# Kernel optimization log

Hardware: AMD Instinct MI355X
Metric: run time of the kernel (lower is better)

## Reference

```python
import jax, jax.numpy as jnp
import numpy as np
from jax import lax


def setup_inputs() -> dict:
    key = jax.random.key(0)
    k1, k2 = jax.random.split(key)
    B, C, H, W = 4, 64, 64, 64
    foreground = jax.random.normal(k1, (B, C, H, W), dtype=jnp.float32)
    masks = jax.random.uniform(k2, (B, 1, H, W), dtype=jnp.float32)
    return {"foreground": foreground, "masks": masks}


def reference(foreground, masks):
    # First-call path of KnowledgeConsistentAttention (att_scores_prev is None).
    # patch_size=3 -> padding=1 around 1x1 dynamic kernels; propagate_size=3 -> 3x3 sum pool.
    B, C, H, W = foreground.shape
    P = H * W
    # Dynamic 1x1 kernels: one per spatial location, L2-normalized over channels.
    K = foreground.reshape(B, C, P).transpose(0, 2, 1)            # [B, P, C]
    norm = jnp.sqrt(jnp.sum(K * K, axis=2, keepdims=True))        # flatten(1).norm per kernel
    K = K / (norm + 1e-8)
    # conv2d with 1x1 kernels and padding=1 == GEMM over zero-padded input.
    Xpad = jnp.pad(foreground, ((0, 0), (0, 0), (1, 1), (1, 1)))  # [B, C, H+2, W+2]
    scores = jnp.einsum('bpc,bchw->bphw', K, Xpad)                # [B, P, H+2, W+2]
    # avg_pool2d(k=3, stride=1, pad=1) * 9 == zero-padded 3x3 sum pool.
    scores = lax.reduce_window(scores, jnp.float32(0.0), lax.add,
                               (1, 1, 3, 3), (1, 1, 1, 1), 'SAME')
    attn = jax.nn.softmax(scores, axis=1)                          # softmax over P kernels
    # conv_transpose2d with 1x1 kernels, padding=1 crops the border back to HxW.
    out = jnp.einsum('bphw,bpc->bchw', attn[:, :, 1:-1, 1:-1], K)  # [B, C, H, W]
    return out
```

## Files before the change

kernel.cpp:

```cpp
#include <hip/hip_runtime.h>
#include <hip/hip_bf16.h>
#include <math.h>

#define Bn 4
#define Cn 64
#define Pn 4096
#define QT 64
#define PBK 128
#define NITER (Pn / PBK)
#define LOG2E 1.4426950408889634f

typedef __attribute__((ext_vector_type(8))) short short8;
typedef __attribute__((ext_vector_type(4))) short short4v;
typedef __attribute__((ext_vector_type(4))) float float4v;
typedef unsigned short bfu;

__device__ __forceinline__ bfu f2bf(float x) {
    unsigned u = __float_as_uint(x);
    u = (u + 0x7fffu + ((u >> 16) & 1u)) >> 16;
    return (bfu)u;
}

__global__ __launch_bounds__(256) void prep_kernel(const float* __restrict__ fg,
                                                   bfu* __restrict__ Kpc,
                                                   bfu* __restrict__ Kcp2,
                                                   float* __restrict__ S) {
    __shared__ float shbuf[64 * 64];
    int t = threadIdx.x;
    if (blockIdx.x < 512) {
        float* tile  = shbuf;
        float* rnorm = shbuf + 64 * 33;
        int b  = blockIdx.x >> 7;
        int p0 = (blockIdx.x & 127) << 5;
        const float* src = fg + (size_t)b * Cn * Pn + p0;
        #pragma unroll
        for (int i = 0; i < 8; ++i) {
            int idx = i * 256 + t;
            int c = idx >> 5, p = idx & 31;
            tile[c * 33 + p] = src[(size_t)c * Pn + p];
        }
        __syncthreads();
        if (t < 32) {
            float ss = 0.f;
            #pragma unroll
            for (int c = 0; c < 64; ++c) { float v = tile[c * 33 + t]; ss += v * v; }
            rnorm[t] = 1.0f / (sqrtf(ss) + 1e-8f);
        }
        __syncthreads();
        bfu* dpc = Kpc + ((size_t)b * Pn + p0) * Cn;
        #pragma unroll
        for (int i = 0; i < 8; ++i) {
            int idx = i * 256 + t;
            int p = idx >> 6, c = idx & 63;
            dpc[(size_t)p * Cn + c] = f2bf(tile[c * 33 + p] * rnorm[p]);
        }
        bfu* d2 = Kcp2 + ((size_t)b * 256 + (p0 >> 4)) * 1024;
        #pragma unroll
        for (int i = 0; i < 8; ++i) {
            int idx = i * 256 + t;
            int c = idx >> 5, p = idx & 31;
            d2[(size_t)(p >> 4) * 1024 + c * 16 + (p & 15)] =
                f2bf(tile[c * 33 + p] * rnorm[p]);
        }
    } else {
        float (*pl)[64] = (float(*)[64])shbuf;
        int bc = blockIdx.x - 512;
        const float* src = fg + (size_t)bc * Pn;
        float*       dst = S  + (size_t)bc * Pn;
        #pragma unroll
        for (int i = 0; i < 16; ++i) {
            int idx = i * 256 + t;
            pl[idx >> 6][idx & 63] = src[idx];
        }
        __syncthreads();
        #pragma unroll
        for (int i = 0; i < 16; ++i) {
            int idx = i * 256 + t;
            int h = idx >> 6, w = idx & 63;
            float s = 0.f;
            #pragma unroll
            for (int dh = -1; dh <= 1; ++dh) {
                int hh = h + dh;
                if (hh < 0 || hh >= 64) continue;
                #pragma unroll
                for (int dw = -1; dw <= 1; ++dw) {
                    int ww = w + dw;
                    if (ww < 0 || ww >= 64) continue;
                    s += pl[hh][ww];
                }
            }
            dst[idx] = s * LOG2E;
        }
    }
}

__global__ __launch_bounds__(512, 1) void flash_kernel(const bfu* __restrict__ Kpc,
                                                       const bfu* __restrict__ Kcp2,
                                                       const float* __restrict__ S,
                                                       float* __restrict__ out) {
    __shared__ __align__(16) bfu smem[33792];
    __shared__ float wredl[8][QT];
    bfu* Sl = smem;

    int i  = blockIdx.x;
    int b  = (i & 7) >> 1;
    int qt = ((i >> 3) << 1) | (i & 1);
    int q0 = qt * QT;
    int t  = threadIdx.x;
    int w = t >> 6, l = t & 63, lq = l & 15, quad = l >> 4;

    const float* Sg  = S    + (size_t)b * Cn * Pn;
    const bfu*   gpc = Kpc  + (size_t)b * Pn * Cn;
    const bfu*   gt  = Kcp2 + (size_t)b * 256 * 1024;

    {
        int c = t >> 3, qq = (t & 7) * 8;
        const float* sp = &Sg[(size_t)c * Pn + q0 + qq];
        float4 v0 = *(const float4*)sp;
        float4 v1 = *(const float4*)(sp + 4);
        float vv[8] = {v0.x, v0.y, v0.z, v0.w, v1.x, v1.y, v1.z, v1.w};
        int ch = c >> 3, cl = c & 7;
        #pragma unroll
        for (int k = 0; k < 8; ++k) {
            int row = qq + k;
            Sl[row * 64 + ((ch ^ (row & 7)) << 3) + cl] = f2bf(vv[k]);
        }
    }
    __syncthreads();

    short8 bs[4][2];
    #pragma unroll
    for (int nt = 0; nt < 4; ++nt)
        #pragma unroll
        for (int ks = 0; ks < 2; ++ks) {
            int row = nt * 16 + lq;
            bs[nt][ks] = *(const short8*)&Sl[row * 64 + (((ks * 4 + quad) ^ (lq & 7)) << 3)];
        }

    float4v o[4][4];
    #pragma unroll
    for (int nt = 0; nt < 4; ++nt)
        #pragma unroll
        for (int cb = 0; cb < 4; ++cb) o[nt][cb] = (float4v){0.f, 0.f, 0.f, 0.f};
    float lacc[4] = {0.f, 0.f, 0.f, 0.f};

    const bfu* ap = gpc + ((size_t)16 * w + lq) * Cn + quad * 8;
    const bfu* tp = gt + (size_t)w * 1024 + lq * 16 + quad * 4;

    float4 a0 = *(const float4*)ap;
    float4 a1 = *(const float4*)(ap + 32);
    short4v kb[4];
    #pragma unroll
    for (int cb = 0; cb < 4; ++cb) kb[cb] = *(const short4v*)(tp + cb * 256);

    for (int pb = 0; pb < NITER; ++pb) {
        float4 na0, na1;
        short4v nkb[4];
        if (pb + 1 < NITER) {
            const bfu* apn = ap + (size_t)(pb + 1) * PBK * Cn;
            na0 = *(const float4*)apn;
            na1 = *(const float4*)(apn + 32);
            const bfu* tpn = tp + (size_t)(pb + 1) * 8 * 1024;
            #pragma unroll
            for (int cb = 0; cb < 4; ++cb) nkb[cb] = *(const short4v*)(tpn + cb * 256);
        }

        short8 af0 = *(short8*)&a0, af1 = *(short8*)&a1;
        float4v sc[4];
        #pragma unroll
        for (int nt = 0; nt < 4; ++nt) {
            float4v acc = (float4v){0.f, 0.f, 0.f, 0.f};
            acc = __builtin_amdgcn_mfma_f32_16x16x32_bf16(af0, bs[nt][0], acc, 0, 0, 0);
            acc = __builtin_amdgcn_mfma_f32_16x16x32_bf16(af1, bs[nt][1], acc, 0, 0, 0);
            sc[nt] = acc;
        }

        short4v epk[4];
        #pragma unroll
        for (int nt = 0; nt < 4; ++nt) {
            float e0 = __builtin_amdgcn_exp2f(sc[nt][0]);
            float e1 = __builtin_amdgcn_exp2f(sc[nt][1]);
            float e2 = __builtin_amdgcn_exp2f(sc[nt][2]);
            float e3 = __builtin_amdgcn_exp2f(sc[nt][3]);
            lacc[nt] += (e0 + e1) + (e2 + e3);
            short4v ep = {(short)f2bf(e0), (short)f2bf(e1), (short)f2bf(e2), (short)f2bf(e3)};
            epk[nt] = ep;
        }

        #pragma unroll
        for (int cb = 0; cb < 4; ++cb) {
            #pragma unroll
            for (int nt = 0; nt < 4; ++nt)
                o[nt][cb] = __builtin_amdgcn_mfma_f32_16x16x16bf16_1k(epk[nt], kb[cb], o[nt][cb], 0, 0, 0);
        }

        a0 = na0; a1 = na1;
        #pragma unroll
        for (int cb = 0; cb < 4; ++cb) kb[cb] = nkb[cb];
    }

    #pragma unroll
    for (int nt = 0; nt < 4; ++nt) {
        lacc[nt] += __shfl_xor(lacc[nt], 16);
        lacc[nt] += __shfl_xor(lacc[nt], 32);
    }
    if (quad == 0)
        #pragma unroll
        for (int nt = 0; nt < 4; ++nt) wredl[w][nt * 16 + lq] = lacc[nt];

    float* Ol = (float*)smem;
    __syncthreads();
    if (w < 4) {
        #pragma unroll
        for (int nt = 0; nt < 4; ++nt)
            #pragma unroll
            for (int cb = 0; cb < 4; ++cb)
                #pragma unroll
                for (int r = 0; r < 4; ++r)
                    Ol[(w * 64 + 16 * cb + lq) * 66 + nt * 16 + quad * 4 + r] = o[nt][cb][r];
    }
    __syncthreads();
    if (w >= 4) {
        #pragma unroll
        for (int nt = 0; nt < 4; ++nt)
            #pragma unroll
            for (int cb = 0; cb < 4; ++cb)
                #pragma unroll
                for (int r = 0; r < 4; ++r)
                    Ol[((w - 4) * 64 + 16 * cb + lq) * 66 + nt * 16 + quad * 4 + r] += o[nt][cb][r];
    }
    __syncthreads();

    float* og = out + (size_t)b * Cn * Pn;
    #pragma unroll
    for (int k = 0; k < 8; ++k) {
        int idx = k * 512 + t;
        int c = idx >> 6, q = idx & 63;
        float lsum = ((wredl[0][q] + wredl[1][q]) + (wredl[2][q] + wredl[3][q])) +
                     ((wredl[4][q] + wredl[5][q]) + (wredl[6][q] + wredl[7][q]));
        float v = ((Ol[c * 66 + q] + Ol[(64 + c) * 66 + q]) +
                   (Ol[(128 + c) * 66 + q] + Ol[(192 + c) * 66 + q])) / lsum;
        og[(size_t)c * Pn + q0 + q] = v;
    }
}

extern "C" void kernel_launch(void* const* d_in, const int* in_sizes, int n_in,
                              void* d_out, int out_size, void* d_ws, size_t ws_size,
                              hipStream_t stream) {
    const float* fg = (const float*)d_in[0];
    float* out = (float*)d_out;
    bfu*   Kpc  = (bfu*)d_ws;
    bfu*   Kcp2 = Kpc + (size_t)Bn * Pn * Cn;
    float* S    = (float*)(Kcp2 + (size_t)Bn * Pn * Cn);

    prep_kernel <<<768, 256, 0, stream>>>(fg, Kpc, Kcp2, S);
    flash_kernel<<<Bn * 64, 512, 0, stream>>>(Kpc, Kcp2, S, out);
}
```

Baseline: 92.42 us.

## Split key dimension across two blocks and combine partial attention outputs

The flash kernel now runs 512 blocks of 256 threads instead of 256 blocks of 512. Each block processes half of the key positions for a query tile and writes unnormalized partial outputs and row sums to workspace. A new combine kernel adds the two halves and normalizes. The goal is more blocks per CU and better occupancy, at the cost of an extra kernel launch and extra global traffic for the partial results.

```diff
diff --git a/kernel.cpp b/kernel.cpp
--- a/kernel.cpp
+++ b/kernel.cpp
@@ -6,8 +6,8 @@
 #define Cn 64
 #define Pn 4096
 #define QT 64
-#define PBK 128
-#define NITER (Pn / PBK)
+#define PBK 64
+#define NITER 32
 #define LOG2E 1.4426950408889634f
 
 typedef __attribute__((ext_vector_type(8))) short short8;
@@ -94,17 +94,19 @@
     }
 }
 
-__global__ __launch_bounds__(512, 1) void flash_kernel(const bfu* __restrict__ Kpc,
+__global__ __launch_bounds__(256, 3) void flash_kernel(const bfu* __restrict__ Kpc,
                                                        const bfu* __restrict__ Kcp2,
                                                        const float* __restrict__ S,
-                                                       float* __restrict__ out) {
-    __shared__ __align__(16) bfu smem[33792];
-    __shared__ float wredl[8][QT];
+                                                       float* __restrict__ Opart,
+                                                       float* __restrict__ Lpart) {
+    __shared__ __align__(16) bfu smem[16896];
+    __shared__ float wredl[4][QT];
     bfu* Sl = smem;
 
     int i  = blockIdx.x;
     int b  = (i & 7) >> 1;
-    int qt = ((i >> 3) << 1) | (i & 1);
+    int ph = i & 1;
+    int qt = i >> 3;
     int q0 = qt * QT;
     int t  = threadIdx.x;
     int w = t >> 6, l = t & 63, lq = l & 15, quad = l >> 4;
@@ -114,16 +116,18 @@
     const bfu*   gt  = Kcp2 + (size_t)b * 256 * 1024;
 
     {
-        int c = t >> 3, qq = (t & 7) * 8;
+        int c = t >> 2, qq = (t & 3) * 16;
         const float* sp = &Sg[(size_t)c * Pn + q0 + qq];
-        float4 v0 = *(const float4*)sp;
-        float4 v1 = *(const float4*)(sp + 4);
-        float vv[8] = {v0.x, v0.y, v0.z, v0.w, v1.x, v1.y, v1.z, v1.w};
         int ch = c >> 3, cl = c & 7;
         #pragma unroll
-        for (int k = 0; k < 8; ++k) {
-            int row = qq + k;
-            Sl[row * 64 + ((ch ^ (row & 7)) << 3) + cl] = f2bf(vv[k]);
+        for (int v4 = 0; v4 < 4; ++v4) {
+            float4 v = *(const float4*)(sp + v4 * 4);
+            float vv[4] = {v.x, v.y, v.z, v.w};
+            #pragma unroll
+            for (int k = 0; k < 4; ++k) {
+                int row = qq + v4 * 4 + k;
+                Sl[row * 64 + ((ch ^ (row & 7)) << 3) + cl] = f2bf(vv[k]);
+            }
         }
     }
     __syncthreads();
@@ -144,8 +148,8 @@
         for (int cb = 0; cb < 4; ++cb) o[nt][cb] = (float4v){0.f, 0.f, 0.f, 0.f};
     float lacc[4] = {0.f, 0.f, 0.f, 0.f};
 
-    const bfu* ap = gpc + ((size_t)16 * w + lq) * Cn + quad * 8;
-    const bfu* tp = gt + (size_t)w * 1024 + lq * 16 + quad * 4;
+    const bfu* ap = gpc + ((size_t)ph * 2048 + 16 * w + lq) * Cn + quad * 8;
+    const bfu* tp = gt + ((size_t)ph * 128 + w) * 1024 + lq * 16 + quad * 4;
 
     float4 a0 = *(const float4*)ap;
     float4 a1 = *(const float4*)(ap + 32);
@@ -160,7 +164,7 @@
             const bfu* apn = ap + (size_t)(pb + 1) * PBK * Cn;
             na0 = *(const float4*)apn;
             na1 = *(const float4*)(apn + 32);
-            const bfu* tpn = tp + (size_t)(pb + 1) * 8 * 1024;
+            const bfu* tpn = tp + (size_t)(pb + 1) * 4 * 1024;
             #pragma unroll
             for (int cb = 0; cb < 4; ++cb) nkb[cb] = *(const short4v*)(tpn + cb * 256);
         }
@@ -210,7 +214,7 @@
 
     float* Ol = (float*)smem;
     __syncthreads();
-    if (w < 4) {
+    if (w < 2) {
         #pragma unroll
         for (int nt = 0; nt < 4; ++nt)
             #pragma unroll
@@ -220,27 +224,48 @@
                     Ol[(w * 64 + 16 * cb + lq) * 66 + nt * 16 + quad * 4 + r] = o[nt][cb][r];
     }
     __syncthreads();
-    if (w >= 4) {
+    if (w >= 2) {
         #pragma unroll
         for (int nt = 0; nt < 4; ++nt)
             #pragma unroll
             for (int cb = 0; cb < 4; ++cb)
                 #pragma unroll
                 for (int r = 0; r < 4; ++r)
-                    Ol[((w - 4) * 64 + 16 * cb + lq) * 66 + nt * 16 + quad * 4 + r] += o[nt][cb][r];
-    }
-    __syncthreads();
-
-    float* og = out + (size_t)b * Cn * Pn;
-    #pragma unroll
-    for (int k = 0; k < 8; ++k) {
-        int idx = k * 512 + t;
+                    Ol[((w - 2) * 64 + 16 * cb + lq) * 66 + nt * 16 + quad * 4 + r] += o[nt][cb][r];
+    }
+    __syncthreads();
+
+    size_t slot = ((size_t)(b * 2 + ph) * 64 + qt);
+    float* Op = Opart + slot * 4096;
+    #pragma unroll
+    for (int k = 0; k < 16; ++k) {
+        int idx = k * 256 + t;
         int c = idx >> 6, q = idx & 63;
-        float lsum = ((wredl[0][q] + wredl[1][q]) + (wredl[2][q] + wredl[3][q])) +
-                     ((wredl[4][q] + wredl[5][q]) + (wredl[6][q] + wredl[7][q]));
-        float v = ((Ol[c * 66 + q] + Ol[(64 + c) * 66 + q]) +
-                   (Ol[(128 + c) * 66 + q] + Ol[(192 + c) * 66 + q])) / lsum;
-        og[(size_t)c * Pn + q0 + q] = v;
+        Op[idx] = Ol[c * 66 + q] + Ol[(64 + c) * 66 + q];
+    }
+    if (t < 64)
+        Lpart[slot * 64 + t] = ((wredl[0][t] + wredl[1][t]) + (wredl[2][t] + wredl[3][t]));
+}
+
+__global__ __launch_bounds__(256) void combine_kernel(const float* __restrict__ Opart,
+                                                      const float* __restrict__ Lpart,
+                                                      float* __restrict__ out) {
+    int i = blockIdx.x;
+    int b = i >> 6, qt = i & 63;
+    size_t s0 = ((size_t)(b * 2 + 0) * 64 + qt);
+    size_t s1 = ((size_t)(b * 2 + 1) * 64 + qt);
+    const float* O0 = Opart + s0 * 4096;
+    const float* O1 = Opart + s1 * 4096;
+    __shared__ float linv[64];
+    int t = threadIdx.x;
+    if (t < 64) linv[t] = 1.0f / (Lpart[s0 * 64 + t] + Lpart[s1 * 64 + t]);
+    __syncthreads();
+    float* og = out + (size_t)b * Cn * Pn + qt * 64;
+    #pragma unroll
+    for (int k = 0; k < 16; ++k) {
+        int idx = k * 256 + t;
+        int c = idx >> 6, q = idx & 63;
+        og[(size_t)c * Pn + q] = (O0[idx] + O1[idx]) * linv[q];
     }
 }
 
@@ -252,7 +277,10 @@
     bfu*   Kpc  = (bfu*)d_ws;
     bfu*   Kcp2 = Kpc + (size_t)Bn * Pn * Cn;
     float* S    = (float*)(Kcp2 + (size_t)Bn * Pn * Cn);
-
-    prep_kernel <<<768, 256, 0, stream>>>(fg, Kpc, Kcp2, S);
-    flash_kernel<<<Bn * 64, 512, 0, stream>>>(Kpc, Kcp2, S, out);
-}
+    float* Opart = S + (size_t)Bn * Cn * Pn;
+    float* Lpart = Opart + (size_t)512 * 4096;
+
+    prep_kernel   <<<768, 256, 0, stream>>>(fg, Kpc, Kcp2, S);
+    flash_kernel  <<<512, 256, 0, stream>>>(Kpc, Kcp2, S, Opart, Lpart);
+    combine_kernel<<<256, 256, 0, stream>>>(Opart, Lpart, out);
+}
```

After: 99.66 us. +7.8%, slower.
